# Kernel optimization log

Hardware: AMD Instinct MI355X
Metric: run time of the kernel (lower is better)

Reference implementation:

```python
import jax, jax.numpy as jnp
import numpy as np

B, S, DM, H, DFF, NL = 4, 1024, 512, 8, 2048, 2
D = DM // H
EPS = 1e-9


def setup_inputs() -> dict:
    key = jax.random.key(0)
    ks = jax.random.split(key, 16)
    x = jax.random.normal(ks[0], (B, S, DM), jnp.float32)
    # padding-style mask: 1.0 where attention is blocked
    pad = (jax.random.uniform(ks[1], (B, S)) < 0.1).astype(jnp.float32)
    mask = jnp.maximum(pad[:, :, None], pad[:, None, :])  # [B,S,S]
    protok = jax.random.randint(ks[2], (B, S), 0, 21).astype(jnp.int32)

    def w(k, fan_in, fan_out):
        lim = np.sqrt(6.0 / (fan_in + fan_out)).astype(np.float32)
        return jax.random.uniform(k, (fan_in, fan_out), jnp.float32, -lim, lim)

    return {
        "x": x, "mask": mask, "protok": protok,
        "wq": w(ks[3], DM, DM), "bq": jnp.zeros((DM,), jnp.float32),
        "wk": w(ks[4], DM, DM), "bk": jnp.zeros((DM,), jnp.float32),
        "wv": w(ks[5], DM, DM), "bv": jnp.zeros((DM,), jnp.float32),
        "wo": w(ks[6], DM, DM), "bo": jnp.zeros((DM,), jnp.float32),
        "w1": w(ks[7], DM, DFF), "b1": jnp.zeros((DFF,), jnp.float32),
        "w2": w(ks[8], DFF, DM), "b2": jnp.zeros((DM,), jnp.float32),
        "ln1_g": jnp.ones((DM,), jnp.float32), "ln1_b": jnp.zeros((DM,), jnp.float32),
        "ln2_g": jnp.ones((DM,), jnp.float32), "ln2_b": jnp.zeros((DM,), jnp.float32),
        "layer_num": NL,
    }


def _layernorm(y, g, b):
    m = jnp.mean(y, axis=-1, keepdims=True)
    v = jnp.mean(jnp.square(y - m), axis=-1, keepdims=True)
    return (y - m) * jax.lax.rsqrt(v + EPS) * g + b


def reference(x, mask, protok, wq, bq, wk, bk, wv, bv, wo, bo,
              w1, b1, w2, b2, ln1_g, ln1_b, ln2_g, ln2_b, layer_num):
    b, s, dm = x.shape
    # count_nonzero(protok[0:1,:]) rescale for the 2D softmax (seq == max_pro_len)
    nz = jnp.count_nonzero(protok[0]).astype(jnp.float32)
    neg = mask[:, None, :, :] * -1e9  # [B,1,S,S] broadcast over heads

    def split(t):  # [B,S,DM] -> [B,H,S,D]
        return t.reshape(b, s, H, D).transpose(0, 2, 1, 3)

    def layer(h):
        q = split(h @ wq + bq)
        k = split(h @ wk + bk)
        v = split(h @ wv + bv)
        logits = jnp.einsum('bhid,bhjd->bhij', q, k) / jnp.sqrt(jnp.float32(D))
        logits = logits + neg
        # 2D softmax jointly over axes (2,3), then rescale by nonzero-token count
        A = jax.nn.softmax(logits.reshape(b, H, s * s), axis=-1).reshape(b, H, s, s) * nz
        # faithful quirk: output = A^T @ v
        o = jnp.einsum('bhji,bhjd->bhid', A, v)
        o = o.transpose(0, 2, 1, 3).reshape(b, s, dm)
        attn_out = o @ wo + bo
        out1 = _layernorm(h + attn_out, ln1_g, ln1_b)
        ffn = jax.nn.relu(out1 @ w1 + b1) @ w2 + b2
        return _layernorm(out1 + ffn, ln2_g, ln2_b)

    # Encoders reuses one shared layer layer_num times (self.rencoder overwritten in loop)
    for _ in range(int(layer_num)):
        x = layer(x)
    return x
```

## Files before the change

kernel.cpp:

```cpp
#include <hip/hip_runtime.h>

typedef unsigned short u16;
typedef __bf16 bf16x8 __attribute__((ext_vector_type(8)));
typedef float f32x4 __attribute__((ext_vector_type(4)));
typedef u16 u16x4 __attribute__((ext_vector_type(4)));

#define LOG2E 1.44269504089f
#define SOFF 16.0f

__device__ __forceinline__ f32x4 mfma16(bf16x8 a, bf16x8 b, f32x4 c) {
    return __builtin_amdgcn_mfma_f32_16x16x32_bf16(a, b, c, 0, 0, 0);
}
__device__ __forceinline__ u16 f2bf(float f) {
    union { float f; unsigned u; } x; x.f = f;
    unsigned r = x.u + 0x7FFFu + ((x.u >> 16) & 1u);
    return (u16)(r >> 16);
}
__device__ __forceinline__ float bf2f(u16 u) {
    union { unsigned u; float f; } x; x.u = ((unsigned)u) << 16;
    return x.f;
}
__device__ __forceinline__ void gload_lds16(const u16* g, u16* l) {
    __builtin_amdgcn_global_load_lds((const __attribute__((address_space(1))) unsigned int*)g,
                                     (__attribute__((address_space(3))) unsigned int*)l, 16, 0, 0);
}


__device__ __forceinline__ void transp_tile(const float* __restrict__ in, u16* __restrict__ out,
                                            int R, int C, int r0, int c0,
                                            float (*t)[33], int tid) {
    const int tx = tid & 31, ty = tid >> 5;
#pragma unroll
    for (int k = 0; k < 4; ++k) t[ty + k * 8][tx] = in[(size_t)(r0 + ty + k * 8) * C + c0 + tx];
    __syncthreads();
#pragma unroll
    for (int k = 0; k < 4; ++k) out[(size_t)(c0 + ty + k * 8) * R + r0 + tx] = f2bf(t[tx][ty + k * 8]);
}

__global__ __launch_bounds__(256) void prep_kernel(
    const float* __restrict__ x,
    const float* __restrict__ wq, const float* __restrict__ wk,
    const float* __restrict__ wv, const float* __restrict__ wo,
    const float* __restrict__ w1, const float* __restrict__ w2,
    const float* __restrict__ mask, const int* __restrict__ protok,
    u16* __restrict__ hbf, u16* __restrict__ wqT, u16* __restrict__ wkT,
    u16* __restrict__ wvT, u16* __restrict__ woT, u16* __restrict__ w1T, u16* __restrict__ w2T,
    float* __restrict__ padneg, float* __restrict__ nzf) {
    __shared__ float t[32][33];
    __shared__ int red[256];
    const int id = blockIdx.x, tid = threadIdx.x;
    if (id < 1024) {
        const int z = id >> 8, rem = id & 255;
        const float* in = z == 0 ? wq : (z == 1 ? wk : (z == 2 ? wv : wo));
        u16* out = z == 0 ? wqT : (z == 1 ? wkT : (z == 2 ? wvT : woT));
        transp_tile(in, out, 512, 512, (rem >> 4) * 32, (rem & 15) * 32, t, tid);
    } else if (id < 2048) {
        const int rem = id - 1024;
        transp_tile(w1, w1T, 512, 2048, (rem >> 6) * 32, (rem & 63) * 32, t, tid);
    } else if (id < 3072) {
        const int rem = id - 2048;
        transp_tile(w2, w2T, 2048, 512, (rem >> 4) * 32, (rem & 15) * 32, t, tid);
    } else if (id < 4096) {
        const int i = ((id - 3072) * 256 + tid) * 8;
        f32x4 a = *(const f32x4*)(x + i);
        f32x4 b = *(const f32x4*)(x + i + 4);
        u16x4 o0, o1;
#pragma unroll
        for (int k = 0; k < 4; ++k) { o0[k] = f2bf(a[k]); o1[k] = f2bf(b[k]); }
        *(u16x4*)(hbf + i) = o0;
        *(u16x4*)(hbf + i + 4) = o1;
    } else if (id == 4096) {
        for (int i = tid; i < 4096; i += 256) {
            const int b = i >> 10, s = i & 1023;
            const float m = mask[(size_t)((b << 10) + s) * 1024 + s];
            padneg[i] = (m > 0.5f) ? -1.5e9f : -SOFF;
        }
    } else {
        int c = 0;
        for (int i = tid; i < 1024; i += 256) c += (protok[i] != 0) ? 1 : 0;
        red[tid] = c;
        __syncthreads();
        for (int s = 128; s > 0; s >>= 1) {
            if (tid < s) red[tid] += red[tid + s];
            __syncthreads();
        }
        if (tid == 0) nzf[0] = (float)red[0];
    }
}

template <int BM, int BN, int MODE>
__global__ __launch_bounds__(256) void gemm_bf16(
    const u16* __restrict__ A,
    const u16* __restrict__ Bt0, const u16* __restrict__ Bt1, const u16* __restrict__ Bt2,
    const float* __restrict__ bias0, const float* __restrict__ bias1, const float* __restrict__ bias2,
    void* __restrict__ dst0, void* __restrict__ dst1, void* __restrict__ dst2,
    const int K, const int N) {
    constexpr int BK = 64;
    constexpr int WM = BM / 2, WN = BN / 2, MI = WM / 16, NI = WN / 16;
    __shared__ u16 lA[BM * BK];
    __shared__ u16 lB[BN * BK];
    const int tid = threadIdx.x;
    const int w = tid >> 6, lane = tid & 63, q = lane >> 4, ln = lane & 15;
    const int wm = w >> 1, wn = w & 1;
    const int n0 = blockIdx.x * BN, m0 = blockIdx.y * BM;
    const int rr = lane >> 3;
    const int cs = ((lane & 7) ^ rr) * 8;

    const u16* Bt;
    const float* bias;
    int nb, sel = 0;
    if (MODE == 0) {
        sel = n0 >> 9;
        Bt = sel == 0 ? Bt0 : (sel == 1 ? Bt1 : Bt2);
        bias = sel == 0 ? bias0 : (sel == 1 ? bias1 : bias2);
        nb = n0 & 511;
    } else {
        Bt = Bt0; bias = bias0; nb = n0;
    }

    const f32x4 vzero = {0.f, 0.f, 0.f, 0.f};
    f32x4 acc[MI][NI];
#pragma unroll
    for (int i = 0; i < MI; ++i)
#pragma unroll
        for (int j = 0; j < NI; ++j) acc[i][j] = vzero;

    const int swa = ln & 7;
    for (int k0 = 0; k0 < K; k0 += BK) {
        const u16* Ag = A + (size_t)m0 * K + k0;
        const u16* Bg = Bt + (size_t)nb * K + k0;
#pragma unroll
        for (int c = 0; c < BM / 32; ++c) {
            const int r = (w * (BM / 32) + c) * 8;
            gload_lds16(Ag + (size_t)(r + rr) * K + cs, &lA[r * BK]);
        }
#pragma unroll
        for (int c = 0; c < BN / 32; ++c) {
            const int r = (w * (BN / 32) + c) * 8;
            gload_lds16(Bg + (size_t)(r + rr) * K + cs, &lB[r * BK]);
        }
        __syncthreads();
#pragma unroll
        for (int kb = 0; kb < 2; ++kb) {
            bf16x8 af[MI], bfr[NI];
#pragma unroll
            for (int mi = 0; mi < MI; ++mi)
                af[mi] = *(const bf16x8*)&lA[(wm * WM + mi * 16 + ln) * BK + ((((kb << 2) + q) ^ swa) << 3)];
#pragma unroll
            for (int ni = 0; ni < NI; ++ni)
                bfr[ni] = *(const bf16x8*)&lB[(wn * WN + ni * 16 + ln) * BK + ((((kb << 2) + q) ^ swa) << 3)];
#pragma unroll
            for (int mi = 0; mi < MI; ++mi)
#pragma unroll
                for (int ni = 0; ni < NI; ++ni) acc[mi][ni] = mfma16(af[mi], bfr[ni], acc[mi][ni]);
        }
        __syncthreads();
    }

    const float scl = (MODE == 0 && sel == 1) ? 0.125f * LOG2E : 1.0f;
#pragma unroll
    for (int mi = 0; mi < MI; ++mi) {
#pragma unroll
        for (int ni = 0; ni < NI; ++ni) {
            const int col = n0 + wn * WN + ni * 16 + ln;
            const float bv = bias[MODE == 0 ? (col & 511) : col];
#pragma unroll
            for (int r = 0; r < 4; ++r) {
                const int row = m0 + wm * WM + mi * 16 + q * 4 + r;
                const float v = (acc[mi][ni][r] + bv) * scl;
                if (MODE == 0) {
                    const int cc = col & 511, hh = cc >> 6, dd = cc & 63;
                    const int bb = row >> 10, ss = row & 1023;
                    if (sel < 2) {
                        u16* dq = (u16*)(sel == 0 ? dst0 : dst1);
                        dq[(((bb << 3) + hh) * 1024 + ss) * 64 + dd] = f2bf(v);
                    } else {
                        ((u16*)dst2)[(((bb << 3) + hh) * 64 + dd) * 1024 + ss] = f2bf(v);
                    }
                } else if (MODE == 1) {
                    ((float*)dst0)[(size_t)row * N + col] = v;
                } else {
                    ((u16*)dst0)[(size_t)row * N + col] = f2bf(fmaxf(v, 0.f));
                }
            }
        }
    }
}

#define PSTR 68
__global__ __launch_bounds__(256) void flash_kernel(
    const u16* __restrict__ Kb, const u16* __restrict__ Qb, const u16* __restrict__ VT,
    const float* __restrict__ padneg,
    u16* __restrict__ Ounc, float* __restrict__ blkZ) {
    __shared__ u16 ldsQ[64 * 64];
    __shared__ u16 ldsV[64 * 64];
    __shared__ u16 P[4][16 * PSTR];
    __shared__ float zred[4];
    const int blk = blockIdx.x, ck = blockIdx.y;
    const int it = blk & 15, bh = blk >> 4, b = bh >> 3;
    const int i0 = it << 6;
    const int tid = threadIdx.x;
    const int w = tid >> 6, lane = tid & 63, q = lane >> 4, ln = lane & 15;

    const u16* Ka = Kb + ((bh << 10) + i0 + (w << 4) + ln) * 64;
    const bf16x8 af0 = *(const bf16x8*)(Ka + q * 8);
    const bf16x8 af1 = *(const bf16x8*)(Ka + 32 + q * 8);
    const u16* Qbase = Qb + (bh << 10) * 64;
    const u16* Vbase = VT + (bh << 6) * 1024;
    const float* pn = padneg + (b << 10);
    float pi[4];
#pragma unroll
    for (int r = 0; r < 4; ++r) pi[r] = pn[i0 + (w << 4) + (q << 2) + r];

    float lsum[4] = {0.f, 0.f, 0.f, 0.f};
    const f32x4 vzero = {0.f, 0.f, 0.f, 0.f};
    f32x4 acc[4] = {vzero, vzero, vzero, vzero};
    u16* Pw = &P[w][0];

    const int srow = lane >> 3;
    const int scol = ((lane & 7) ^ srow) * 8;
    const int sw = ln & 7;
    const int half = w & 1;

    for (int js = 0; js < 4; ++js) {
        const int j0 = (ck << 8) + (js << 6);
        if (w < 2) {
            const u16* src = Qbase + (size_t)(j0 + half * 32) * 64;
#pragma unroll
            for (int c = 0; c < 4; ++c) {
                const int r = half * 32 + c * 8;
                gload_lds16(src + (size_t)(c * 8 + srow) * 64 + scol, &ldsQ[r * 64]);
            }
        } else {
            const u16* src = Vbase + (size_t)(half * 32) * 1024 + j0;
#pragma unroll
            for (int c = 0; c < 4; ++c) {
                const int r = half * 32 + c * 8;
                gload_lds16(src + (size_t)(c * 8 + srow) * 1024 + scol, &ldsV[r * 64]);
            }
        }
        __syncthreads();
#pragma unroll
        for (int jt = 0; jt < 4; ++jt) {
            const int jr = (jt << 4) + ln;
            const float pj = pn[j0 + jr];
            bf16x8 b0 = *(const bf16x8*)&ldsQ[jr * 64 + ((q ^ sw) << 3)];
            bf16x8 b1 = *(const bf16x8*)&ldsQ[jr * 64 + (((q + 4) ^ sw) << 3)];
            f32x4 c = vzero;
            c = mfma16(af0, b0, c);
            c = mfma16(af1, b1, c);
#pragma unroll
            for (int r = 0; r < 4; ++r) {
                const float pe = exp2f(c[r] + fminf(pi[r], pj));
                lsum[r] += pe;
                Pw[((q << 2) + r) * PSTR + (jt << 4) + ln] = f2bf(pe);
            }
        }
        const bf16x8 pa0 = *(const bf16x8*)(Pw + ln * PSTR + q * 8);
        const bf16x8 pa1 = *(const bf16x8*)(Pw + ln * PSTR + 32 + q * 8);
#pragma unroll
        for (int ds = 0; ds < 4; ++ds) {
            const int vr = (ds << 4) + ln;
            bf16x8 v0 = *(const bf16x8*)&ldsV[vr * 64 + ((q ^ sw) << 3)];
            bf16x8 v1 = *(const bf16x8*)&ldsV[vr * 64 + (((q + 4) ^ sw) << 3)];
            acc[ds] = mfma16(pa0, v0, acc[ds]);
            acc[ds] = mfma16(pa1, v1, acc[ds]);
        }
        __syncthreads();
    }
    const int t = (bh << 10) + i0 + (w << 4) + (q << 2);
    u16* Oc = Ounc + ((size_t)ck << 21);
#pragma unroll
    for (int ds = 0; ds < 4; ++ds)
#pragma unroll
        for (int r = 0; r < 4; ++r) Oc[(size_t)(t + r) * 64 + (ds << 4) + ln] = f2bf(acc[ds][r]);
    float s = (lsum[0] + lsum[1]) + (lsum[2] + lsum[3]);
#pragma unroll
    for (int o = 1; o < 64; o <<= 1) s += __shfl_xor(s, o);
    if (lane == 0) zred[w] = s;
    __syncthreads();
    if (tid == 0) blkZ[(ck << 9) + blk] = (zred[0] + zred[1]) + (zred[2] + zred[3]);
}

__global__ __launch_bounds__(64) void combine_z(
    const float* __restrict__ blkZ, const float* __restrict__ nzf, float* __restrict__ Zs) {
    const int bh = blockIdx.x, tid = threadIdx.x;
    float v = blkZ[((tid >> 4) << 9) + (bh << 4) + (tid & 15)];
#pragma unroll
    for (int o = 1; o < 64; o <<= 1) v += __shfl_xor(v, o);
    if (tid == 0) Zs[bh] = nzf[0] / v;
}

__global__ __launch_bounds__(256) void scale_o(
    const u16* __restrict__ Ounc, const float* __restrict__ Zs, u16* __restrict__ obf) {
    const int t = blockIdx.x * 4 + (threadIdx.x >> 6);
    const int lane = threadIdx.x & 63;
    const int bh = t >> 10, i = t & 1023, b = bh >> 3, h = bh & 7;
    const float fac = Zs[bh];
    float v = 0.f;
#pragma unroll
    for (int c = 0; c < 4; ++c) v += bf2f(Ounc[((size_t)c << 21) + (size_t)t * 64 + lane]);
    obf[((b << 10) + i) * 512 + (h << 6) + lane] = f2bf(v * fac);
}

__global__ __launch_bounds__(256) void ln_kernel(
    const float* __restrict__ base, const float* __restrict__ delta,
    const float* __restrict__ g, const float* __restrict__ bb,
    float* __restrict__ of32, u16* __restrict__ obf) {
    const int t = blockIdx.x * 4 + (threadIdx.x >> 6);
    const int lane = threadIdx.x & 63;
    const int off = t * 512 + lane * 8;
    f32x4 a0 = *(const f32x4*)(base + off);
    f32x4 a1 = *(const f32x4*)(base + off + 4);
    f32x4 e0 = *(const f32x4*)(delta + off);
    f32x4 e1 = *(const f32x4*)(delta + off + 4);
    float v[8];
#pragma unroll
    for (int k = 0; k < 4; ++k) { v[k] = a0[k] + e0[k]; v[k + 4] = a1[k] + e1[k]; }
    float s = 0.f;
#pragma unroll
    for (int k = 0; k < 8; ++k) s += v[k];
#pragma unroll
    for (int o = 32; o > 0; o >>= 1) s += __shfl_xor(s, o);
    const float mean = s * (1.f / 512.f);
    float vs = 0.f;
#pragma unroll
    for (int k = 0; k < 8; ++k) { const float d = v[k] - mean; vs += d * d; }
#pragma unroll
    for (int o = 32; o > 0; o >>= 1) vs += __shfl_xor(vs, o);
    const float r = rsqrtf(vs * (1.f / 512.f) + 1e-9f);
    f32x4 y0, y1;
    u16x4 o0, o1;
#pragma unroll
    for (int k = 0; k < 4; ++k) {
        const int c = lane * 8 + k;
        const float ya = (v[k] - mean) * r * g[c] + bb[c];
        y0[k] = ya; o0[k] = f2bf(ya);
        const int c2 = c + 4;
        const float yb = (v[k + 4] - mean) * r * g[c2] + bb[c2];
        y1[k] = yb; o1[k] = f2bf(yb);
    }
    *(f32x4*)(of32 + off) = y0;
    *(f32x4*)(of32 + off + 4) = y1;
    *(u16x4*)(obf + off) = o0;
    *(u16x4*)(obf + off + 4) = o1;
}


extern "C" void kernel_launch(void* const* d_in, const int* in_sizes, int n_in,
                              void* d_out, int out_size, void* d_ws, size_t ws_size,
                              hipStream_t stream) {
    const float* x = (const float*)d_in[0];
    const float* mask = (const float*)d_in[1];
    const int* protok = (const int*)d_in[2];
    const float* wq = (const float*)d_in[3]; const float* bq = (const float*)d_in[4];
    const float* wk = (const float*)d_in[5]; const float* bk = (const float*)d_in[6];
    const float* wv = (const float*)d_in[7]; const float* bv = (const float*)d_in[8];
    const float* wo = (const float*)d_in[9]; const float* bo = (const float*)d_in[10];
    const float* w1 = (const float*)d_in[11]; const float* b1 = (const float*)d_in[12];
    const float* w2 = (const float*)d_in[13]; const float* b2 = (const float*)d_in[14];
    const float* ln1g = (const float*)d_in[15]; const float* ln1b = (const float*)d_in[16];
    const float* ln2g = (const float*)d_in[17]; const float* ln2b = (const float*)d_in[18];

    char* p = (char*)d_ws;
    auto take = [&](size_t bytes) -> char* {
        char* r = p;
        p += (bytes + 255) & ~(size_t)255;
        return r;
    };
    u16* wqT = (u16*)take(512 * 512 * 2);
    u16* wkT = (u16*)take(512 * 512 * 2);
    u16* wvT = (u16*)take(512 * 512 * 2);
    u16* woT = (u16*)take(512 * 512 * 2);
    u16* w1T = (u16*)take(2048 * 512 * 2);
    u16* w2T = (u16*)take(512 * 2048 * 2);
    u16* hbf = (u16*)take(4096 * 512 * 2);
    float* hf32 = (float*)take(4096 * 512 * 4);
    u16* qb = (u16*)take(32 * 1024 * 64 * 2);
    u16* kb = (u16*)take(32 * 1024 * 64 * 2);
    u16* vT = (u16*)take(32 * 64 * 1024 * 2);
    u16* Ounc = (u16*)take(4ull * 32 * 1024 * 64 * 2);
    float* blkZ = (float*)take(2048 * 4);
    float* Zs = (float*)take(64 * 4);
    float* nzf = (float*)take(256);
    float* padneg = (float*)take(4096 * 4);
    u16* obf = (u16*)take(4096 * 512 * 2);
    float* attn = (float*)take(4096 * 512 * 4);
    float* out1f = (float*)take(4096 * 512 * 4);
    u16* out1bf = (u16*)take(4096 * 512 * 2);
    u16* f1 = (u16*)take(4096 * 2048 * 2);
    float* ffn = attn;

    prep_kernel<<<dim3(4098), 256, 0, stream>>>(
        x, wq, wk, wv, wo, w1, w2, mask, protok,
        hbf, wqT, wkT, wvT, woT, w1T, w2T, padneg, nzf);

    const float* hin = x;
    for (int l = 0; l < 2; ++l) {
        gemm_bf16<128, 64, 0><<<dim3(24, 32), 256, 0, stream>>>(
            hbf, wqT, wkT, wvT, bq, bk, bv, qb, kb, vT, 512, 1536);
        flash_kernel<<<dim3(512, 4), 256, 0, stream>>>(kb, qb, vT, padneg, Ounc, blkZ);
        combine_z<<<dim3(32), 64, 0, stream>>>(blkZ, nzf, Zs);
        scale_o<<<dim3(8192), 256, 0, stream>>>(Ounc, Zs, obf);
        gemm_bf16<64, 64, 1><<<dim3(8, 64), 256, 0, stream>>>(
            obf, woT, woT, woT, bo, bo, bo, attn, attn, attn, 512, 512);
        ln_kernel<<<dim3(1024), 256, 0, stream>>>(hin, attn, ln1g, ln1b, out1f, out1bf);
        gemm_bf16<128, 128, 2><<<dim3(16, 32), 256, 0, stream>>>(
            out1bf, w1T, w1T, w1T, b1, b1, b1, f1, f1, f1, 512, 2048);
        gemm_bf16<64, 64, 1><<<dim3(8, 64), 256, 0, stream>>>(
            f1, w2T, w2T, w2T, b2, b2, b2, ffn, ffn, ffn, 2048, 512);
        float* hout = (l == 1) ? (float*)d_out : hf32;
        ln_kernel<<<dim3(1024), 256, 0, stream>>>(out1f, ffn, ln2g, ln2b, hout, hbf);
        hin = hf32;
    }
}
```

Measured before the change: 338.2 us.

## Double flash tile rows per block, fold Z combine into scale, remap GEMM blocks

Each flash block now processes 128 query rows (two 64-row sub-tiles), so every staged Q/V tile in LDS is reused twice, and the grid is halved. The combine_z kernel is removed: scale_o reduces the per-block partial sums itself, saving one launch per layer at the cost of a small redundant reduction in every block. GEMM blocks are remapped with a grouped, XCD-aware swizzle of block IDs to improve L2 locality. Both the grouped mapping and the doubled per-thread accumulators (more registers, fewer blocks) can change occupancy.

Result: no change. 340.7 us (+0.7%).

```diff
diff --git a/kernel.cpp b/kernel.cpp
--- a/kernel.cpp
+++ b/kernel.cpp
@@ -24,7 +24,6 @@
     __builtin_amdgcn_global_load_lds((const __attribute__((address_space(1))) unsigned int*)g,
                                      (__attribute__((address_space(3))) unsigned int*)l, 16, 0, 0);
 }
-
 
 __device__ __forceinline__ void transp_tile(const float* __restrict__ in, u16* __restrict__ out,
                                             int R, int C, int r0, int c0,
@@ -102,7 +101,12 @@
     const int tid = threadIdx.x;
     const int w = tid >> 6, lane = tid & 63, q = lane >> 4, ln = lane & 15;
     const int wm = w >> 1, wn = w & 1;
-    const int n0 = blockIdx.x * BN, m0 = blockIdx.y * BM;
+    const int id = blockIdx.y * gridDim.x + blockIdx.x;
+    const int mper = gridDim.y >> 3;
+    const int rest = id >> 3;
+    const int by = (id & 7) * mper + (rest % mper);
+    const int bx = rest / mper;
+    const int n0 = bx * BN, m0 = by * BM;
     const int rr = lane >> 3;
     const int cs = ((lane & 7) ^ rr) * 8;
 
@@ -197,24 +201,32 @@
     __shared__ u16 P[4][16 * PSTR];
     __shared__ float zred[4];
     const int blk = blockIdx.x, ck = blockIdx.y;
-    const int it = blk & 15, bh = blk >> 4, b = bh >> 3;
-    const int i0 = it << 6;
+    const int ig = blk & 7, bh = blk >> 3, b = bh >> 3;
+    const int i0 = ig << 7;
     const int tid = threadIdx.x;
     const int w = tid >> 6, lane = tid & 63, q = lane >> 4, ln = lane & 15;
 
-    const u16* Ka = Kb + ((bh << 10) + i0 + (w << 4) + ln) * 64;
-    const bf16x8 af0 = *(const bf16x8*)(Ka + q * 8);
-    const bf16x8 af1 = *(const bf16x8*)(Ka + 32 + q * 8);
+    bf16x8 af[2][2];
+    float pi[2][4];
+    const float* pn = padneg + (b << 10);
+#pragma unroll
+    for (int it = 0; it < 2; ++it) {
+        const u16* Ka = Kb + ((bh << 10) + i0 + (it << 6) + (w << 4) + ln) * 64;
+        af[it][0] = *(const bf16x8*)(Ka + q * 8);
+        af[it][1] = *(const bf16x8*)(Ka + 32 + q * 8);
+#pragma unroll
+        for (int r = 0; r < 4; ++r) pi[it][r] = pn[i0 + (it << 6) + (w << 4) + (q << 2) + r];
+    }
     const u16* Qbase = Qb + (bh << 10) * 64;
     const u16* Vbase = VT + (bh << 6) * 1024;
-    const float* pn = padneg + (b << 10);
-    float pi[4];
-#pragma unroll
-    for (int r = 0; r < 4; ++r) pi[r] = pn[i0 + (w << 4) + (q << 2) + r];
-
-    float lsum[4] = {0.f, 0.f, 0.f, 0.f};
+
+    float lsum[2][4] = {{0.f, 0.f, 0.f, 0.f}, {0.f, 0.f, 0.f, 0.f}};
     const f32x4 vzero = {0.f, 0.f, 0.f, 0.f};
-    f32x4 acc[4] = {vzero, vzero, vzero, vzero};
+    f32x4 acc[2][4];
+#pragma unroll
+    for (int it = 0; it < 2; ++it)
+#pragma unroll
+        for (int ds = 0; ds < 4; ++ds) acc[it][ds] = vzero;
     u16* Pw = &P[w][0];
 
     const int srow = lane >> 3;
@@ -241,62 +253,72 @@
         }
         __syncthreads();
 #pragma unroll
-        for (int jt = 0; jt < 4; ++jt) {
-            const int jr = (jt << 4) + ln;
-            const float pj = pn[j0 + jr];
-            bf16x8 b0 = *(const bf16x8*)&ldsQ[jr * 64 + ((q ^ sw) << 3)];
-            bf16x8 b1 = *(const bf16x8*)&ldsQ[jr * 64 + (((q + 4) ^ sw) << 3)];
-            f32x4 c = vzero;
-            c = mfma16(af0, b0, c);
-            c = mfma16(af1, b1, c);
-#pragma unroll
-            for (int r = 0; r < 4; ++r) {
-                const float pe = exp2f(c[r] + fminf(pi[r], pj));
-                lsum[r] += pe;
-                Pw[((q << 2) + r) * PSTR + (jt << 4) + ln] = f2bf(pe);
+        for (int it = 0; it < 2; ++it) {
+#pragma unroll
+            for (int jt = 0; jt < 4; ++jt) {
+                const int jr = (jt << 4) + ln;
+                const float pj = pn[j0 + jr];
+                bf16x8 b0 = *(const bf16x8*)&ldsQ[jr * 64 + ((q ^ sw) << 3)];
+                bf16x8 b1 = *(const bf16x8*)&ldsQ[jr * 64 + (((q + 4) ^ sw) << 3)];
+                f32x4 c = vzero;
+                c = mfma16(af[it][0], b0, c);
+                c = mfma16(af[it][1], b1, c);
+#pragma unroll
+                for (int r = 0; r < 4; ++r) {
+                    const float pe = exp2f(c[r] + fminf(pi[it][r], pj));
+                    lsum[it][r] += pe;
+                    Pw[((q << 2) + r) * PSTR + (jt << 4) + ln] = f2bf(pe);
+                }
             }
-        }
-        const bf16x8 pa0 = *(const bf16x8*)(Pw + ln * PSTR + q * 8);
-        const bf16x8 pa1 = *(const bf16x8*)(Pw + ln * PSTR + 32 + q * 8);
-#pragma unroll
-        for (int ds = 0; ds < 4; ++ds) {
-            const int vr = (ds << 4) + ln;
-            bf16x8 v0 = *(const bf16x8*)&ldsV[vr * 64 + ((q ^ sw) << 3)];
-            bf16x8 v1 = *(const bf16x8*)&ldsV[vr * 64 + (((q + 4) ^ sw) << 3)];
-            acc[ds] = mfma16(pa0, v0, acc[ds]);
-            acc[ds] = mfma16(pa1, v1, acc[ds]);
+            const bf16x8 pa0 = *(const bf16x8*)(Pw + ln * PSTR + q * 8);
+            const bf16x8 pa1 = *(const bf16x8*)(Pw + ln * PSTR + 32 + q * 8);
+#pragma unroll
+            for (int ds = 0; ds < 4; ++ds) {
+                const int vr = (ds << 4) + ln;
+                bf16x8 v0 = *(const bf16x8*)&ldsV[vr * 64 + ((q ^ sw) << 3)];
+                bf16x8 v1 = *(const bf16x8*)&ldsV[vr * 64 + (((q + 4) ^ sw) << 3)];
+                acc[it][ds] = mfma16(pa0, v0, acc[it][ds]);
+                acc[it][ds] = mfma16(pa1, v1, acc[it][ds]);
+            }
         }
         __syncthreads();
     }
-    const int t = (bh << 10) + i0 + (w << 4) + (q << 2);
     u16* Oc = Ounc + ((size_t)ck << 21);
 #pragma unroll
-    for (int ds = 0; ds < 4; ++ds)
-#pragma unroll
-        for (int r = 0; r < 4; ++r) Oc[(size_t)(t + r) * 64 + (ds << 4) + ln] = f2bf(acc[ds][r]);
-    float s = (lsum[0] + lsum[1]) + (lsum[2] + lsum[3]);
+    for (int it = 0; it < 2; ++it) {
+        const int t = (bh << 10) + i0 + (it << 6) + (w << 4) + (q << 2);
+#pragma unroll
+        for (int ds = 0; ds < 4; ++ds)
+#pragma unroll
+            for (int r = 0; r < 4; ++r) Oc[(size_t)(t + r) * 64 + (ds << 4) + ln] = f2bf(acc[it][ds][r]);
+    }
+    float s = (lsum[0][0] + lsum[0][1]) + (lsum[0][2] + lsum[0][3]) +
+              (lsum[1][0] + lsum[1][1]) + (lsum[1][2] + lsum[1][3]);
 #pragma unroll
     for (int o = 1; o < 64; o <<= 1) s += __shfl_xor(s, o);
     if (lane == 0) zred[w] = s;
     __syncthreads();
-    if (tid == 0) blkZ[(ck << 9) + blk] = (zred[0] + zred[1]) + (zred[2] + zred[3]);
-}
-
-__global__ __launch_bounds__(64) void combine_z(
-    const float* __restrict__ blkZ, const float* __restrict__ nzf, float* __restrict__ Zs) {
-    const int bh = blockIdx.x, tid = threadIdx.x;
-    float v = blkZ[((tid >> 4) << 9) + (bh << 4) + (tid & 15)];
-#pragma unroll
-    for (int o = 1; o < 64; o <<= 1) v += __shfl_xor(v, o);
-    if (tid == 0) Zs[bh] = nzf[0] / v;
+    if (tid == 0) blkZ[(ck << 8) + blk] = (zred[0] + zred[1]) + (zred[2] + zred[3]);
 }
 
 __global__ __launch_bounds__(256) void scale_o(
-    const u16* __restrict__ Ounc, const float* __restrict__ Zs, u16* __restrict__ obf) {
-    const int t = blockIdx.x * 4 + (threadIdx.x >> 6);
-    const int lane = threadIdx.x & 63;
-    const int bh = t >> 10, i = t & 1023, b = bh >> 3, h = bh & 7;
-    const float fac = Zs[bh];
+    const u16* __restrict__ Ounc, const float* __restrict__ blkZ, const float* __restrict__ nzf,
+    u16* __restrict__ obf) {
+    __shared__ float zsh;
+    const int t0 = blockIdx.x * 4;
+    const int bh = t0 >> 10;
+    const int tid = threadIdx.x;
+    if (tid < 32) {
+        float v = blkZ[((tid >> 3) << 8) + (bh << 3) + (tid & 7)];
+#pragma unroll
+        for (int o = 1; o < 32; o <<= 1) v += __shfl_xor(v, o);
+        if (tid == 0) zsh = nzf[0] / v;
+    }
+    __syncthreads();
+    const float fac = zsh;
+    const int t = t0 + (tid >> 6);
+    const int lane = tid & 63;
+    const int i = t & 1023, b = bh >> 3, h = bh & 7;
     float v = 0.f;
 #pragma unroll
     for (int c = 0; c < 4; ++c) v += bf2f(Ounc[((size_t)c << 21) + (size_t)t * 64 + lane]);
@@ -380,8 +402,7 @@
     u16* kb = (u16*)take(32 * 1024 * 64 * 2);
     u16* vT = (u16*)take(32 * 64 * 1024 * 2);
     u16* Ounc = (u16*)take(4ull * 32 * 1024 * 64 * 2);
-    float* blkZ = (float*)take(2048 * 4);
-    float* Zs = (float*)take(64 * 4);
+    float* blkZ = (float*)take(1024 * 4);
     float* nzf = (float*)take(256);
     float* padneg = (float*)take(4096 * 4);
     u16* obf = (u16*)take(4096 * 512 * 2);
@@ -399,9 +420,8 @@
     for (int l = 0; l < 2; ++l) {
         gemm_bf16<128, 64, 0><<<dim3(24, 32), 256, 0, stream>>>(
             hbf, wqT, wkT, wvT, bq, bk, bv, qb, kb, vT, 512, 1536);
-        flash_kernel<<<dim3(512, 4), 256, 0, stream>>>(kb, qb, vT, padneg, Ounc, blkZ);
-        combine_z<<<dim3(32), 64, 0, stream>>>(blkZ, nzf, Zs);
-        scale_o<<<dim3(8192), 256, 0, stream>>>(Ounc, Zs, obf);
+        flash_kernel<<<dim3(256, 4), 256, 0, stream>>>(kb, qb, vT, padneg, Ounc, blkZ);
+        scale_o<<<dim3(8192), 256, 0, stream>>>(Ounc, blkZ, nzf, obf);
         gemm_bf16<64, 64, 1><<<dim3(8, 64), 256, 0, stream>>>(
             obf, woT, woT, woT, bo, bo, bo, attn, attn, attn, 512, 512);
         ln_kernel<<<dim3(1024), 256, 0, stream>>>(hin, attn, ln1g, ln1b, out1f, out1bf);
```
